# Kernel tuning notes

Hardware: AMD Instinct MI355X
Metric: run time of the kernel (lower is better)

Reference implementation:

```python
import jax, jax.numpy as jnp
import numpy as np

# model dims
V, D, C, H, NL, E, EH = 32000, 256, 2, 8, 2, 8, 1024
B, S = 16, 512
DH = D // H
N = B * S


def _pos_encoding(length, d):
    pos = jnp.arange(length)[:, None].astype(jnp.float32)
    div = jnp.exp(jnp.arange(0, d, 2).astype(jnp.float32) * (-np.log(10000.0) / d))
    pe = jnp.zeros((length, d), dtype=jnp.float32)
    pe = pe.at[:, 0::2].set(jnp.sin(pos * div))
    pe = pe.at[:, 1::2].set(jnp.cos(pos * div))
    return pe


def _ln(x, g, b, eps=1e-5):
    mu = x.mean(-1, keepdims=True)
    var = ((x - mu) ** 2).mean(-1, keepdims=True)
    return (x - mu) / jnp.sqrt(var + eps) * g + b


def setup_inputs():
    key = jax.random.key(0)
    ks = jax.random.split(key, 12)
    n = lambda k, shape, s=0.02: (jax.random.normal(k, shape) * s).astype(jnp.float32)
    return dict(
        x=jax.random.randint(ks[0], (B, S), 0, V),
        emb=n(ks[1], (V, D), 0.1),
        in_proj_w=n(ks[2], (NL, 3 * D, D)),
        in_proj_b=jnp.zeros((NL, 3 * D), jnp.float32),
        out_proj_w=n(ks[3], (NL, D, D)),
        out_proj_b=jnp.zeros((NL, D), jnp.float32),
        ln1_g=jnp.ones((NL, D), jnp.float32), ln1_b=jnp.zeros((NL, D), jnp.float32),
        ln2_g=jnp.ones((NL, D), jnp.float32), ln2_b=jnp.zeros((NL, D), jnp.float32),
        gate_w=n(ks[4], (NL, E, D)), gate_b=jnp.zeros((NL, E), jnp.float32),
        w1=n(ks[5], (NL, E, EH, D)), b1=jnp.zeros((NL, E, EH), jnp.float32),
        w2=n(ks[6], (NL, E, D, EH)), b2=jnp.zeros((NL, E, D), jnp.float32),
        fc1_w=n(ks[7], (128, D), 0.1), fc1_b=jnp.zeros((128,), jnp.float32),
        fc2_w=n(ks[8], (C, 128), 0.1), fc2_b=jnp.zeros((C,), jnp.float32),
    )


def reference(x, emb, in_proj_w, in_proj_b, out_proj_w, out_proj_b,
              ln1_g, ln1_b, ln2_g, ln2_b, gate_w, gate_b,
              w1, b1, w2, b2, fc1_w, fc1_b, fc2_w, fc2_b):
    h = emb[x] * np.sqrt(float(D))                       # [B,S,D]
    h = h + _pos_encoding(S, D)[None]
    pad = h.sum(-1) == 0                                 # key padding mask [B,S]
    for l in range(NL):
        # --- multi-head self-attention ---
        qkv = h @ in_proj_w[l].T + in_proj_b[l]          # [B,S,3D]
        q, k, v = jnp.split(qkv, 3, axis=-1)
        q = q.reshape(B, S, H, DH).transpose(0, 2, 1, 3)
        k = k.reshape(B, S, H, DH).transpose(0, 2, 1, 3)
        v = v.reshape(B, S, H, DH).transpose(0, 2, 1, 3)
        sc = jnp.einsum('bhqd,bhkd->bhqk', q, k) / np.sqrt(float(DH))
        sc = jnp.where(pad[:, None, None, :], -1e9, sc)
        a = jax.nn.softmax(sc, axis=-1)
        ctx = jnp.einsum('bhqk,bhkd->bhqd', a, v).transpose(0, 2, 1, 3).reshape(B, S, D)
        attn_out = ctx @ out_proj_w[l].T + out_proj_b[l]
        h = _ln(h + attn_out, ln1_g[l], ln1_b[l])
        # --- top-1 MoE ---
        xf = h.reshape(N, D)
        gwt = jax.nn.softmax(xf @ gate_w[l].T + gate_b[l], axis=-1)  # [N,E]
        top_idx = jnp.argmax(gwt, axis=-1)                # [N]
        top_w = jnp.max(gwt, axis=-1)                     # [N]
        eh = jax.nn.relu(jnp.einsum('nd,ehd->enh', xf, w1[l]) + b1[l][:, None, :])
        ey = jnp.einsum('enh,edh->end', eh, w2[l]) + b2[l][:, None, :]  # [E,N,D]
        sel = ey[top_idx, jnp.arange(N)]                  # gather routed expert output [N,D]
        moe = (top_w[:, None] * sel).reshape(B, S, D)
        h = _ln(h + moe, ln2_g[l], ln2_b[l])
    m = (~pad)[..., None].astype(h.dtype)                 # [B,S,1]
    pooled = (h * m).sum(1) / jnp.clip(m.sum(1), 1.0)     # masked mean pool [B,D]
    z = jax.nn.relu(pooled @ fc1_w.T + fc1_b)
    return z @ fc2_w.T + fc2_b                            # [B,C]
```

## Files before the change

kernel.cpp:

```cpp
#include <hip/hip_runtime.h>
#include <math.h>

#define D_MODEL 256
#define NTOK    8192
#define SEQ     512
#define NB      16
#define NH      8
#define DHEAD   32
#define NE      8
#define EHID    1024
#define CSTRIDE 32

typedef __attribute__((ext_vector_type(8))) short short8;
typedef __attribute__((ext_vector_type(4))) float floatx4;
typedef unsigned short ushort_t;

__device__ __forceinline__ ushort_t bf16r(float f) {
    unsigned int u = __float_as_uint(f);
    u += 0x7fffu + ((u >> 16) & 1u);
    return (ushort_t)(u >> 16);
}
__device__ __forceinline__ float bf2f(ushort_t b) {
    return __uint_as_float(((unsigned)b) << 16);
}

__global__ __launch_bounds__(256) void wconv(
    const float* __restrict__ src, ushort_t* __restrict__ dst, int n)
{
    const int i = (blockIdx.x * 256 + threadIdx.x) * 4;
    if (i < n) {
        float4 v = *(const float4*)(src + i);
        ushort_t o[4] = { bf16r(v.x), bf16r(v.y), bf16r(v.z), bf16r(v.w) };
        *(uint2*)(dst + i) = *(uint2*)o;
    }
}

__global__ __launch_bounds__(256) void embed_kernel(
    const int* __restrict__ x, const float* __restrict__ emb,
    float* __restrict__ h, ushort_t* __restrict__ hb, int* __restrict__ pad)
{
    __shared__ float wred[4];
    const int n = blockIdx.x;
    const int d = threadIdx.x;
    const int wave = d >> 6;
    const int s = n & (SEQ - 1);
    const int tok = x[n];
    float v = emb[tok * D_MODEL + d] * 16.0f;
    const int j = d >> 1;
    const float c = -9.210340371976184f / 256.0f;
    const float div = expf((float)(2 * j) * c);
    const float ang = (float)s * div;
    v += (d & 1) ? cosf(ang) : sinf(ang);
    h[n * D_MODEL + d] = v;
    hb[n * D_MODEL + d] = bf16r(v);
    float sm = v;
    for (int o = 1; o < 64; o <<= 1) sm += __shfl_xor(sm, o);
    if ((d & 63) == 0) wred[wave] = sm;
    __syncthreads();
    if (d == 0) pad[n] = ((wred[0] + wred[1] + wred[2] + wred[3]) == 0.0f) ? 1 : 0;
}

#define GF_RELU    1
#define GF_OUTBF16 2
#define GF_GATHER  4
#define GF_SCATTER 8

__global__ __launch_bounds__(256) void mfma_gemm(
    const ushort_t* __restrict__ A, const ushort_t* __restrict__ Bw,
    const float* __restrict__ bias, void* __restrict__ Cout,
    int M, int N, int K,
    const int* __restrict__ counts,
    const int* __restrict__ perm, const float* __restrict__ topw,
    int flags)
{
    __shared__ ushort_t As[64][72];
    __shared__ ushort_t Bs[64][72];
    const int e = blockIdx.z;
    int cnt, off = 0;
    if (counts) {
        cnt = counts[e * CSTRIDE];
        if ((int)blockIdx.y * 64 >= cnt) return;
        for (int i = 0; i < e; i++) off += counts[i * CSTRIDE];
    } else { cnt = M; }
    const ushort_t* Bp = Bw + (size_t)e * N * K;
    const float* bp = bias + (size_t)e * N;
    const int m0 = blockIdx.y * 64, n0 = blockIdx.x * 64;
    const int tid = threadIdx.x;
    const int sr0 = tid >> 3;
    const int kc0 = (tid & 7) * 8;
    const int r0 = m0 + sr0, r1 = r0 + 32;
    const bool v0 = r0 < cnt, v1 = r1 < cnt;
    size_t a0, a1;
    if (flags & GF_GATHER) {
        a0 = (size_t)perm[off + (v0 ? r0 : 0)];
        a1 = (size_t)perm[off + (v1 ? r1 : 0)];
    } else {
        a0 = (size_t)(off + (v0 ? r0 : 0));
        a1 = (size_t)(off + (v1 ? r1 : 0));
    }
    const ushort_t* Ap0 = A + a0 * K + kc0;
    const ushort_t* Ap1 = A + a1 * K + kc0;
    const ushort_t* Bp0 = Bp + (size_t)(n0 + sr0) * K + kc0;
    const ushort_t* Bp1 = Bp + (size_t)(n0 + sr0 + 32) * K + kc0;
    const int lane = tid & 63, wave = tid >> 6;
    const int wm = (wave & 1) * 32, wn = (wave >> 1) * 32;
    const int fr = lane & 15, fk = (lane >> 4) * 8;
    floatx4 acc[2][2];
#pragma unroll
    for (int i = 0; i < 2; i++)
#pragma unroll
        for (int jj = 0; jj < 2; jj++) acc[i][jj] = (floatx4){0.f, 0.f, 0.f, 0.f};

    for (int k0 = 0; k0 < K; k0 += 64) {
        uint4 av0 = *(const uint4*)(Ap0 + k0);
        uint4 av1 = *(const uint4*)(Ap1 + k0);
        uint4 bv0 = *(const uint4*)(Bp0 + k0);
        uint4 bv1 = *(const uint4*)(Bp1 + k0);
        __syncthreads();
        *(uint4*)&As[sr0][kc0]      = av0;
        *(uint4*)&As[sr0 + 32][kc0] = av1;
        *(uint4*)&Bs[sr0][kc0]      = bv0;
        *(uint4*)&Bs[sr0 + 32][kc0] = bv1;
        __syncthreads();
#pragma unroll
        for (int ks = 0; ks < 2; ks++) {
            const int ko = ks * 32 + fk;
            short8 fa0 = *(const short8*)&As[wm + fr][ko];
            short8 fa1 = *(const short8*)&As[wm + 16 + fr][ko];
            short8 fb0 = *(const short8*)&Bs[wn + fr][ko];
            short8 fb1 = *(const short8*)&Bs[wn + 16 + fr][ko];
            acc[0][0] = __builtin_amdgcn_mfma_f32_16x16x32_bf16(fa0, fb0, acc[0][0], 0, 0, 0);
            acc[0][1] = __builtin_amdgcn_mfma_f32_16x16x32_bf16(fa0, fb1, acc[0][1], 0, 0, 0);
            acc[1][0] = __builtin_amdgcn_mfma_f32_16x16x32_bf16(fa1, fb0, acc[1][0], 0, 0, 0);
            acc[1][1] = __builtin_amdgcn_mfma_f32_16x16x32_bf16(fa1, fb1, acc[1][1], 0, 0, 0);
        }
    }
    const int crow0 = (lane >> 4) * 4;
    const int ccol = lane & 15;
#pragma unroll
    for (int fm = 0; fm < 2; fm++) {
#pragma unroll
        for (int fn = 0; fn < 2; fn++) {
            const int gcol = n0 + wn + fn * 16 + ccol;
            const float bsv = bp[gcol];
#pragma unroll
            for (int r = 0; r < 4; r++) {
                const int grow = m0 + wm + fm * 16 + crow0 + r;
                if (grow >= cnt) continue;
                float v = acc[fm][fn][r] + bsv;
                if (flags & GF_RELU) v = fmaxf(v, 0.f);
                if (flags & GF_SCATTER) {
                    const int tok = perm[off + grow];
                    ((float*)Cout)[(size_t)tok * N + gcol] = v * topw[tok];
                } else if (flags & GF_OUTBF16) {
                    ((ushort_t*)Cout)[(size_t)(off + grow) * N + gcol] = bf16r(v);
                } else {
                    ((float*)Cout)[(size_t)(off + grow) * N + gcol] = v;
                }
            }
        }
    }
}

__global__ __launch_bounds__(256) void attn_kernel(
    const ushort_t* __restrict__ qkvb, const int* __restrict__ pad,
    ushort_t* __restrict__ ctxb)
{
    __shared__ ushort_t Kt[64 * 40];
    __shared__ ushort_t Vt[32 * 72];
    __shared__ ushort_t Ps[64 * 72];
    __shared__ float padf[512];
    const int tid = threadIdx.x;
    const int lane = tid & 63;
    const int wave = tid >> 6;
    const int quad = lane >> 4;
    const int l16  = lane & 15;
    const int bid = blockIdx.x;
    const int qt = bid & 7;
    const int hh = (bid >> 3) & 7;
    const int b = bid >> 6;
    const int q0 = wave * 16;

    padf[tid]       = (float)pad[b * SEQ + tid];
    padf[tid + 256] = (float)pad[b * SEQ + 256 + tid];

    short8 qfrag = *(const short8*)(qkvb +
        (size_t)(b * SEQ + qt * 64 + q0 + l16) * 768 + hh * 32 + quad * 8);

    const int skey = tid >> 2;
    const int schunk = (tid & 3) * 8;

    floatx4 o0 = {0.f,0.f,0.f,0.f}, o1 = {0.f,0.f,0.f,0.f};
    float lsum[4] = {0.f, 0.f, 0.f, 0.f};
    const float scale = 0.17677669529663687f;

    for (int t = 0; t < 8; t++) {
        const int kbase = b * SEQ + t * 64;
        __syncthreads();
        uint4 kv = *(const uint4*)(qkvb + (size_t)(kbase + skey) * 768 + 256 + hh * 32 + schunk);
        *(uint4*)&Kt[skey * 40 + schunk] = kv;
        uint4 vv = *(const uint4*)(qkvb + (size_t)(kbase + skey) * 768 + 512 + hh * 32 + schunk);
        ushort_t vs[8]; *(uint4*)vs = vv;
#pragma unroll
        for (int j = 0; j < 8; j++) {
            const int d = schunk + j;
            Vt[d * 72 + (skey ^ ((d >> 3) << 3))] = vs[j];
        }
        __syncthreads();
        floatx4 sfr[4];
#pragma unroll
        for (int fn = 0; fn < 4; fn++) {
            short8 kf = *(const short8*)&Kt[(fn * 16 + l16) * 40 + quad * 8];
            sfr[fn] = __builtin_amdgcn_mfma_f32_16x16x32_bf16(
                qfrag, kf, (floatx4){0.f,0.f,0.f,0.f}, 0, 0, 0);
        }
#pragma unroll
        for (int fn = 0; fn < 4; fn++) {
            const int keyl = fn * 16 + l16;
            const float pv = padf[t * 64 + keyl];
#pragma unroll
            for (int r = 0; r < 4; r++) {
                float p = (pv != 0.f) ? 0.f : __expf(sfr[fn][r] * scale);
                ushort_t pb = bf16r(p);
                lsum[r] += bf2f(pb);
                Ps[(q0 + quad * 4 + r) * 72 + keyl] = pb;
            }
        }
#pragma unroll
        for (int kc = 0; kc < 2; kc++) {
            short8 pf = *(const short8*)&Ps[(q0 + l16) * 72 + kc * 32 + quad * 8];
            {
                const int d = l16;
                short8 vf = *(const short8*)&Vt[d * 72 + ((kc * 32 + quad * 8) ^ ((d >> 3) << 3))];
                o0 = __builtin_amdgcn_mfma_f32_16x16x32_bf16(pf, vf, o0, 0, 0, 0);
            }
            {
                const int d = 16 + l16;
                short8 vf = *(const short8*)&Vt[d * 72 + ((kc * 32 + quad * 8) ^ ((d >> 3) << 3))];
                o1 = __builtin_amdgcn_mfma_f32_16x16x32_bf16(pf, vf, o1, 0, 0, 0);
            }
        }
    }
#pragma unroll
    for (int r = 0; r < 4; r++) {
        float v = lsum[r];
        v += __shfl_xor(v, 1); v += __shfl_xor(v, 2);
        v += __shfl_xor(v, 4); v += __shfl_xor(v, 8);
        lsum[r] = 1.f / v;
    }
    const int nq = b * SEQ + qt * 64 + q0 + quad * 4;
#pragma unroll
    for (int r = 0; r < 4; r++) {
        ushort_t* outp = ctxb + (size_t)(nq + r) * 256 + hh * 32;
        outp[l16]      = bf16r(o0[r] * lsum[r]);
        outp[16 + l16] = bf16r(o1[r] * lsum[r]);
    }
}

__global__ __launch_bounds__(256) void add_ln(
    float* __restrict__ h, const float* __restrict__ add,
    const float* __restrict__ g, const float* __restrict__ b,
    ushort_t* __restrict__ hb)
{
    __shared__ float wred[8];
    const int n = blockIdx.x;
    const int d = threadIdx.x;
    const int wave = d >> 6;
    const float v = h[n * D_MODEL + d] + add[n * D_MODEL + d];
    float s = v;
    for (int o = 1; o < 64; o <<= 1) s += __shfl_xor(s, o);
    if ((d & 63) == 0) wred[wave] = s;
    __syncthreads();
    const float mu = (wred[0] + wred[1] + wred[2] + wred[3]) * (1.0f / 256.0f);
    const float c = v - mu;
    float cs = c * c;
    for (int o = 1; o < 64; o <<= 1) cs += __shfl_xor(cs, o);
    if ((d & 63) == 0) wred[4 + wave] = cs;
    __syncthreads();
    const float var = (wred[4] + wred[5] + wred[6] + wred[7]) * (1.0f / 256.0f);
    const float o = c * rsqrtf(var + 1e-5f) * g[d] + b[d];
    h[n * D_MODEL + d] = o;
    hb[n * D_MODEL + d] = bf16r(o);
}

__global__ __launch_bounds__(256) void gate_kernel(
    const float* __restrict__ h, const float* __restrict__ gw,
    const float* __restrict__ gb, int* __restrict__ top_idx,
    float* __restrict__ top_w, int* __restrict__ pos, int* __restrict__ counts)
{
    __shared__ int lidx[128];
    __shared__ int lpos[128];
    __shared__ int hist[NE];
    __shared__ int base[NE];
    const int wave = threadIdx.x >> 6;
    const int lane = threadIdx.x & 63;
    const int t0 = blockIdx.x * 128 + wave * 32;
    float4 gwr[NE];
#pragma unroll
    for (int e = 0; e < NE; e++)
        gwr[e] = *(const float4*)&gw[e * D_MODEL + lane * 4];
    float gbr[NE];
#pragma unroll
    for (int e = 0; e < NE; e++) gbr[e] = gb[e];

    for (int i = 0; i < 32; i++) {
        const int n = t0 + i;
        float4 hv = *(const float4*)&h[(size_t)n * D_MODEL + lane * 4];
        float lg[NE];
#pragma unroll
        for (int e = 0; e < NE; e++)
            lg[e] = hv.x * gwr[e].x + hv.y * gwr[e].y + hv.z * gwr[e].z + hv.w * gwr[e].w;
#pragma unroll
        for (int e = 0; e < NE; e++) {
            float v = lg[e];
            for (int o = 1; o < 64; o <<= 1) v += __shfl_xor(v, o);
            lg[e] = v;
        }
        if (lane == 0) {
            float best = -1e30f; int bi = 0;
#pragma unroll
            for (int e = 0; e < NE; e++) {
                lg[e] += gbr[e];
                if (lg[e] > best) { best = lg[e]; bi = e; }
            }
            float ssum = 0.0f;
#pragma unroll
            for (int e = 0; e < NE; e++) ssum += __expf(lg[e] - best);
            top_idx[n] = bi;
            top_w[n] = 1.0f / ssum;
            lidx[wave * 32 + i] = bi;
        }
    }
    __syncthreads();
    if (threadIdx.x < NE) hist[threadIdx.x] = 0;
    __syncthreads();
    if (threadIdx.x < 128)
        lpos[threadIdx.x] = atomicAdd(&hist[lidx[threadIdx.x]], 1);
    __syncthreads();
    if (threadIdx.x < NE)
        base[threadIdx.x] = atomicAdd(&counts[threadIdx.x * CSTRIDE], hist[threadIdx.x]);
    __syncthreads();
    if (threadIdx.x < 128)
        pos[blockIdx.x * 128 + threadIdx.x] = base[lidx[threadIdx.x]] + lpos[threadIdx.x];
}

__global__ __launch_bounds__(256) void scatter_perm(
    const int* __restrict__ top_idx, const int* __restrict__ pos,
    const int* __restrict__ counts, int* __restrict__ perm)
{
    __shared__ int offs_s[NE];
    if (threadIdx.x < NE) {
        int a = 0;
        for (int i = 0; i < (int)threadIdx.x; i++) a += counts[i * CSTRIDE];
        offs_s[threadIdx.x] = a;
    }
    __syncthreads();
    const int n = blockIdx.x * 256 + threadIdx.x;
    if (n < NTOK) perm[offs_s[top_idx[n]] + pos[n]] = n;
}

__global__ __launch_bounds__(256) void pool1(
    const float* __restrict__ h, const int* __restrict__ pad,
    float* __restrict__ pooled, float* __restrict__ cntb)
{
    const int b = blockIdx.x, c = blockIdx.y, d = threadIdx.x;
    float s = 0.0f; int cnt = 0;
    for (int i = 0; i < 32; i++) {
        const int idx = b * SEQ + c * 32 + i;
        if (!pad[idx]) { s += h[(size_t)idx * D_MODEL + d]; cnt++; }
    }
    atomicAdd(&pooled[b * D_MODEL + d], s);
    if (d == 0) atomicAdd(&cntb[b], (float)cnt);
}

__global__ __launch_bounds__(128) void cls_kernel(
    const float* __restrict__ pooled, const float* __restrict__ cntb,
    const float* __restrict__ fc1w, const float* __restrict__ fc1b,
    const float* __restrict__ fc2w, const float* __restrict__ fc2b,
    float* __restrict__ out)
{
    __shared__ float zs[128];
    const int b = blockIdx.x;
    const int j = threadIdx.x;
    const float invc = 1.0f / fmaxf(cntb[b], 1.0f);
    float s = 0.0f;
    for (int d = 0; d < D_MODEL; d++) s += pooled[b * D_MODEL + d] * fc1w[j * D_MODEL + d];
    zs[j] = fmaxf(s * invc + fc1b[j], 0.0f);
    __syncthreads();
    if (j < 2) {
        float o = fc2b[j];
        for (int i = 0; i < 128; i++) o += zs[i] * fc2w[j * 128 + i];
        out[b * 2 + j] = o;
    }
}

extern "C" void kernel_launch(void* const* d_in, const int* in_sizes, int n_in,
                              void* d_out, int out_size, void* d_ws, size_t ws_size,
                              hipStream_t stream)
{
    const int*   x          = (const int*)d_in[0];
    const float* emb        = (const float*)d_in[1];
    const float* in_proj_w  = (const float*)d_in[2];
    const float* in_proj_b  = (const float*)d_in[3];
    const float* out_proj_w = (const float*)d_in[4];
    const float* out_proj_b = (const float*)d_in[5];
    const float* ln1_g      = (const float*)d_in[6];
    const float* ln1_b      = (const float*)d_in[7];
    const float* ln2_g      = (const float*)d_in[8];
    const float* ln2_b      = (const float*)d_in[9];
    const float* gate_w     = (const float*)d_in[10];
    const float* gate_b     = (const float*)d_in[11];
    const float* w1         = (const float*)d_in[12];
    const float* b1         = (const float*)d_in[13];
    const float* w2         = (const float*)d_in[14];
    const float* b2         = (const float*)d_in[15];
    const float* fc1_w      = (const float*)d_in[16];
    const float* fc1_b      = (const float*)d_in[17];
    const float* fc2_w      = (const float*)d_in[18];
    const float* fc2_b      = (const float*)d_in[19];
    float* out = (float*)d_out;

    float* ws = (float*)d_ws;
    float*    h      = ws;
    float*    tmp    = ws + 2097152;
    ushort_t* qkvb   = (ushort_t*)(ws + 4194304);
    ushort_t* ctxb   = (ushort_t*)(ws + 7340032);
    ushort_t* ehb    = (ushort_t*)(ws + 4194304);
    ushort_t* hb     = (ushort_t*)(ws + 8388608);
    ushort_t* wb     = (ushort_t*)(ws + 9437184);
    float*    top_w  = ws + 10485760;
    float*    pooled = ws + 10493952;
    float*    cntb   = ws + 10498048;
    int* ipart   = (int*)(ws + 10498064);
    int* pad     = ipart;
    int* top_idx = ipart + 8192;
    int* pos     = ipart + 16384;
    int* perm    = ipart + 24576;
    int* counts  = ipart + 32768;

    embed_kernel<<<NTOK, 256, 0, stream>>>(x, emb, h, hb, pad);
    hipMemsetAsync(pooled, 0, (NB * D_MODEL + NB) * sizeof(float), stream);

    for (int l = 0; l < 2; l++) {
        wconv<<<192, 256, 0, stream>>>(in_proj_w + (size_t)l * 196608, wb, 196608);
        mfma_gemm<<<dim3(768 / 64, NTOK / 64, 1), 256, 0, stream>>>(
            hb, wb, in_proj_b + l * 768, qkvb, NTOK, 768, 256,
            nullptr, nullptr, nullptr, GF_OUTBF16);
        attn_kernel<<<NB * NH * (SEQ / 64), 256, 0, stream>>>(qkvb, pad, ctxb);
        wconv<<<64, 256, 0, stream>>>(out_proj_w + (size_t)l * 65536, wb, 65536);
        mfma_gemm<<<dim3(256 / 64, NTOK / 64, 1), 256, 0, stream>>>(
            ctxb, wb, out_proj_b + l * 256, tmp, NTOK, 256, 256,
            nullptr, nullptr, nullptr, 0);
        add_ln<<<NTOK, 256, 0, stream>>>(h, tmp, ln1_g + l * 256, ln1_b + l * 256, hb);
        hipMemsetAsync(counts, 0, NE * CSTRIDE * sizeof(int), stream);
        gate_kernel<<<NTOK / 128, 256, 0, stream>>>(
            h, gate_w + l * NE * 256, gate_b + l * NE, top_idx, top_w, pos, counts);
        scatter_perm<<<NTOK / 256, 256, 0, stream>>>(top_idx, pos, counts, perm);
        wconv<<<2048, 256, 0, stream>>>(w1 + (size_t)l * 2097152, wb, 2097152);
        mfma_gemm<<<dim3(EHID / 64, NTOK / 64, NE), 256, 0, stream>>>(
            hb, wb, b1 + l * NE * EHID, ehb, 0, EHID, 256,
            counts, perm, nullptr, GF_GATHER | GF_RELU | GF_OUTBF16);
        wconv<<<2048, 256, 0, stream>>>(w2 + (size_t)l * 2097152, wb, 2097152);
        mfma_gemm<<<dim3(D_MODEL / 64, NTOK / 64, NE), 256, 0, stream>>>(
            ehb, wb, b2 + l * NE * 256, tmp, 0, D_MODEL, 1024,
            counts, perm, top_w, GF_SCATTER);
        add_ln<<<NTOK, 256, 0, stream>>>(h, tmp, ln2_g + l * 256, ln2_b + l * 256, hb);
    }

    pool1<<<dim3(NB, 16), 256, 0, stream>>>(h, pad, pooled, cntb);
    cls_kernel<<<NB, 128, 0, stream>>>(pooled, cntb, fc1_w, fc1_b, fc2_w, fc2_b, out);
}
```

Baseline: 466.9 us.

## Batch all weight conversions into one launch and enlarge GEMM tiles

All bf16 weight conversions for both layers are merged into one kernel launched at the start, replacing eight small per-GEMM conversion launches that each reused a shared scratch buffer. The MFMA GEMM becomes a template on tile size, and every GEMM now uses 128x128 or 128x64 tiles, so each wave computes more fragments. Larger tiles cut global-load traffic per FLOP and the number of launches, at the cost of more registers and LDS per block, fewer blocks (the QKV GEMM gets 384 blocks), and more wasted rows in sparse expert tiles.

```diff
diff --git a/kernel.cpp b/kernel.cpp
--- a/kernel.cpp
+++ b/kernel.cpp
@@ -24,15 +24,20 @@
     return __uint_as_float(((unsigned)b) << 16);
 }
 
-__global__ __launch_bounds__(256) void wconv(
-    const float* __restrict__ src, ushort_t* __restrict__ dst, int n)
-{
-    const int i = (blockIdx.x * 256 + threadIdx.x) * 4;
-    if (i < n) {
-        float4 v = *(const float4*)(src + i);
-        ushort_t o[4] = { bf16r(v.x), bf16r(v.y), bf16r(v.z), bf16r(v.w) };
-        *(uint2*)(dst + i) = *(uint2*)o;
-    }
+__global__ __launch_bounds__(256) void wconv_all(
+    const float* __restrict__ in_proj_w, const float* __restrict__ out_proj_w,
+    const float* __restrict__ w1, const float* __restrict__ w2,
+    ushort_t* __restrict__ wball)
+{
+    const int g = blockIdx.x * 256 + threadIdx.x;
+    const float* src; ushort_t* dst; int lo;
+    if (g < 98304)        { src = in_proj_w;  dst = wball;           lo = g; }
+    else if (g < 131072)  { src = out_proj_w; dst = wball + 393216;  lo = g - 98304; }
+    else if (g < 1179648) { src = w1;         dst = wball + 524288;  lo = g - 131072; }
+    else                  { src = w2;         dst = wball + 4718592; lo = g - 1179648; }
+    float4 v = *(const float4*)(src + (size_t)lo * 4);
+    ushort_t o[4] = { bf16r(v.x), bf16r(v.y), bf16r(v.z), bf16r(v.w) };
+    *(uint2*)(dst + (size_t)lo * 4) = *(uint2*)o;
 }
 
 __global__ __launch_bounds__(256) void embed_kernel(
@@ -65,7 +70,8 @@
 #define GF_GATHER  4
 #define GF_SCATTER 8
 
-__global__ __launch_bounds__(256) void mfma_gemm(
+template<int BM, int BN>
+__global__ __launch_bounds__(256) void gemm_t(
     const ushort_t* __restrict__ A, const ushort_t* __restrict__ Bw,
     const float* __restrict__ bias, void* __restrict__ Cout,
     int M, int N, int K,
@@ -73,81 +79,84 @@
     const int* __restrict__ perm, const float* __restrict__ topw,
     int flags)
 {
-    __shared__ ushort_t As[64][72];
-    __shared__ ushort_t Bs[64][72];
+    constexpr int MI = BM / 32;
+    constexpr int NI = BN / 32;
+    constexpr int MF = BM / 32;
+    constexpr int NF = BN / 32;
+    __shared__ ushort_t As[BM][72];
+    __shared__ ushort_t Bs[BN][72];
     const int e = blockIdx.z;
     int cnt, off = 0;
     if (counts) {
         cnt = counts[e * CSTRIDE];
-        if ((int)blockIdx.y * 64 >= cnt) return;
+        if ((int)blockIdx.y * BM >= cnt) return;
         for (int i = 0; i < e; i++) off += counts[i * CSTRIDE];
     } else { cnt = M; }
     const ushort_t* Bp = Bw + (size_t)e * N * K;
     const float* bp = bias + (size_t)e * N;
-    const int m0 = blockIdx.y * 64, n0 = blockIdx.x * 64;
+    const int m0 = blockIdx.y * BM, n0 = blockIdx.x * BN;
     const int tid = threadIdx.x;
-    const int sr0 = tid >> 3;
-    const int kc0 = (tid & 7) * 8;
-    const int r0 = m0 + sr0, r1 = r0 + 32;
-    const bool v0 = r0 < cnt, v1 = r1 < cnt;
-    size_t a0, a1;
-    if (flags & GF_GATHER) {
-        a0 = (size_t)perm[off + (v0 ? r0 : 0)];
-        a1 = (size_t)perm[off + (v1 ? r1 : 0)];
-    } else {
-        a0 = (size_t)(off + (v0 ? r0 : 0));
-        a1 = (size_t)(off + (v1 ? r1 : 0));
-    }
-    const ushort_t* Ap0 = A + a0 * K + kc0;
-    const ushort_t* Ap1 = A + a1 * K + kc0;
-    const ushort_t* Bp0 = Bp + (size_t)(n0 + sr0) * K + kc0;
-    const ushort_t* Bp1 = Bp + (size_t)(n0 + sr0 + 32) * K + kc0;
+    const int srow = tid >> 3;
+    const int kc = (tid & 7) * 8;
+    size_t arow[MI];
+#pragma unroll
+    for (int i = 0; i < MI; i++) {
+        const int r = m0 + i * 32 + srow;
+        const bool v = r < cnt;
+        if (flags & GF_GATHER) arow[i] = (size_t)perm[off + (v ? r : 0)];
+        else                   arow[i] = (size_t)(off + (v ? r : 0));
+    }
     const int lane = tid & 63, wave = tid >> 6;
-    const int wm = (wave & 1) * 32, wn = (wave >> 1) * 32;
+    const int wm = (wave & 1) * (BM / 2), wn = (wave >> 1) * (BN / 2);
     const int fr = lane & 15, fk = (lane >> 4) * 8;
-    floatx4 acc[2][2];
-#pragma unroll
-    for (int i = 0; i < 2; i++)
-#pragma unroll
-        for (int jj = 0; jj < 2; jj++) acc[i][jj] = (floatx4){0.f, 0.f, 0.f, 0.f};
+    floatx4 acc[MF][NF];
+#pragma unroll
+    for (int i = 0; i < MF; i++)
+#pragma unroll
+        for (int jj = 0; jj < NF; jj++) acc[i][jj] = (floatx4){0.f, 0.f, 0.f, 0.f};
 
     for (int k0 = 0; k0 < K; k0 += 64) {
-        uint4 av0 = *(const uint4*)(Ap0 + k0);
-        uint4 av1 = *(const uint4*)(Ap1 + k0);
-        uint4 bv0 = *(const uint4*)(Bp0 + k0);
-        uint4 bv1 = *(const uint4*)(Bp1 + k0);
+        uint4 av[MI], bv[NI];
+#pragma unroll
+        for (int i = 0; i < MI; i++)
+            av[i] = *(const uint4*)(A + arow[i] * K + k0 + kc);
+#pragma unroll
+        for (int i = 0; i < NI; i++)
+            bv[i] = *(const uint4*)(Bp + (size_t)(n0 + i * 32 + srow) * K + k0 + kc);
         __syncthreads();
-        *(uint4*)&As[sr0][kc0]      = av0;
-        *(uint4*)&As[sr0 + 32][kc0] = av1;
-        *(uint4*)&Bs[sr0][kc0]      = bv0;
-        *(uint4*)&Bs[sr0 + 32][kc0] = bv1;
+#pragma unroll
+        for (int i = 0; i < MI; i++) *(uint4*)&As[i * 32 + srow][kc] = av[i];
+#pragma unroll
+        for (int i = 0; i < NI; i++) *(uint4*)&Bs[i * 32 + srow][kc] = bv[i];
         __syncthreads();
 #pragma unroll
         for (int ks = 0; ks < 2; ks++) {
             const int ko = ks * 32 + fk;
-            short8 fa0 = *(const short8*)&As[wm + fr][ko];
-            short8 fa1 = *(const short8*)&As[wm + 16 + fr][ko];
-            short8 fb0 = *(const short8*)&Bs[wn + fr][ko];
-            short8 fb1 = *(const short8*)&Bs[wn + 16 + fr][ko];
-            acc[0][0] = __builtin_amdgcn_mfma_f32_16x16x32_bf16(fa0, fb0, acc[0][0], 0, 0, 0);
-            acc[0][1] = __builtin_amdgcn_mfma_f32_16x16x32_bf16(fa0, fb1, acc[0][1], 0, 0, 0);
-            acc[1][0] = __builtin_amdgcn_mfma_f32_16x16x32_bf16(fa1, fb0, acc[1][0], 0, 0, 0);
-            acc[1][1] = __builtin_amdgcn_mfma_f32_16x16x32_bf16(fa1, fb1, acc[1][1], 0, 0, 0);
+            short8 fa[MF], fb[NF];
+#pragma unroll
+            for (int m = 0; m < MF; m++) fa[m] = *(const short8*)&As[wm + m * 16 + fr][ko];
+#pragma unroll
+            for (int n = 0; n < NF; n++) fb[n] = *(const short8*)&Bs[wn + n * 16 + fr][ko];
+#pragma unroll
+            for (int m = 0; m < MF; m++)
+#pragma unroll
+                for (int n = 0; n < NF; n++)
+                    acc[m][n] = __builtin_amdgcn_mfma_f32_16x16x32_bf16(fa[m], fb[n], acc[m][n], 0, 0, 0);
         }
     }
     const int crow0 = (lane >> 4) * 4;
     const int ccol = lane & 15;
 #pragma unroll
-    for (int fm = 0; fm < 2; fm++) {
-#pragma unroll
-        for (int fn = 0; fn < 2; fn++) {
-            const int gcol = n0 + wn + fn * 16 + ccol;
+    for (int m = 0; m < MF; m++) {
+#pragma unroll
+        for (int n = 0; n < NF; n++) {
+            const int gcol = n0 + wn + n * 16 + ccol;
             const float bsv = bp[gcol];
 #pragma unroll
             for (int r = 0; r < 4; r++) {
-                const int grow = m0 + wm + fm * 16 + crow0 + r;
+                const int grow = m0 + wm + m * 16 + crow0 + r;
                 if (grow >= cnt) continue;
-                float v = acc[fm][fn][r] + bsv;
+                float v = acc[m][n][r] + bsv;
                 if (flags & GF_RELU) v = fmaxf(v, 0.f);
                 if (flags & GF_SCATTER) {
                     const int tok = perm[off + grow];
@@ -427,7 +436,6 @@
     ushort_t* ctxb   = (ushort_t*)(ws + 7340032);
     ushort_t* ehb    = (ushort_t*)(ws + 4194304);
     ushort_t* hb     = (ushort_t*)(ws + 8388608);
-    ushort_t* wb     = (ushort_t*)(ws + 9437184);
     float*    top_w  = ws + 10485760;
     float*    pooled = ws + 10493952;
     float*    cntb   = ws + 10498048;
@@ -437,32 +445,35 @@
     int* pos     = ipart + 16384;
     int* perm    = ipart + 24576;
     int* counts  = ipart + 32768;
-
+    ushort_t* wball = (ushort_t*)(ws + 10531088);
+
+    wconv_all<<<8704, 256, 0, stream>>>(in_proj_w, out_proj_w, w1, w2, wball);
     embed_kernel<<<NTOK, 256, 0, stream>>>(x, emb, h, hb, pad);
     hipMemsetAsync(pooled, 0, (NB * D_MODEL + NB) * sizeof(float), stream);
 
     for (int l = 0; l < 2; l++) {
-        wconv<<<192, 256, 0, stream>>>(in_proj_w + (size_t)l * 196608, wb, 196608);
-        mfma_gemm<<<dim3(768 / 64, NTOK / 64, 1), 256, 0, stream>>>(
-            hb, wb, in_proj_b + l * 768, qkvb, NTOK, 768, 256,
+        const ushort_t* inb_l  = wball + (size_t)l * 196608;
+        const ushort_t* outb_l = wball + 393216 + (size_t)l * 65536;
+        const ushort_t* w1b_l  = wball + 524288 + (size_t)l * 2097152;
+        const ushort_t* w2b_l  = wball + 4718592 + (size_t)l * 2097152;
+
+        gemm_t<128, 128><<<dim3(768 / 128, NTOK / 128, 1), 256, 0, stream>>>(
+            hb, inb_l, in_proj_b + l * 768, qkvb, NTOK, 768, 256,
             nullptr, nullptr, nullptr, GF_OUTBF16);
         attn_kernel<<<NB * NH * (SEQ / 64), 256, 0, stream>>>(qkvb, pad, ctxb);
-        wconv<<<64, 256, 0, stream>>>(out_proj_w + (size_t)l * 65536, wb, 65536);
-        mfma_gemm<<<dim3(256 / 64, NTOK / 64, 1), 256, 0, stream>>>(
-            ctxb, wb, out_proj_b + l * 256, tmp, NTOK, 256, 256,
+        gemm_t<128, 64><<<dim3(256 / 64, NTOK / 128, 1), 256, 0, stream>>>(
+            ctxb, outb_l, out_proj_b + l * 256, tmp, NTOK, 256, 256,
             nullptr, nullptr, nullptr, 0);
         add_ln<<<NTOK, 256, 0, stream>>>(h, tmp, ln1_g + l * 256, ln1_b + l * 256, hb);
         hipMemsetAsync(counts, 0, NE * CSTRIDE * sizeof(int), stream);
         gate_kernel<<<NTOK / 128, 256, 0, stream>>>(
             h, gate_w + l * NE * 256, gate_b + l * NE, top_idx, top_w, pos, counts);
         scatter_perm<<<NTOK / 256, 256, 0, stream>>>(top_idx, pos, counts, perm);
-        wconv<<<2048, 256, 0, stream>>>(w1 + (size_t)l * 2097152, wb, 2097152);
-        mfma_gemm<<<dim3(EHID / 64, NTOK / 64, NE), 256, 0, stream>>>(
-            hb, wb, b1 + l * NE * EHID, ehb, 0, EHID, 256,
+        gemm_t<128, 128><<<dim3(EHID / 128, NTOK / 128, NE), 256, 0, stream>>>(
+            hb, w1b_l, b1 + l * NE * EHID, ehb, 0, EHID, 256,
             counts, perm, nullptr, GF_GATHER | GF_RELU | GF_OUTBF16);
-        wconv<<<2048, 256, 0, stream>>>(w2 + (size_t)l * 2097152, wb, 2097152);
-        mfma_gemm<<<dim3(D_MODEL / 64, NTOK / 64, NE), 256, 0, stream>>>(
-            ehb, wb, b2 + l * NE * 256, tmp, 0, D_MODEL, 1024,
+        gemm_t<128, 64><<<dim3(D_MODEL / 64, NTOK / 128, NE), 256, 0, stream>>>(
+            ehb, w2b_l, b2 + l * NE * 256, tmp, 0, D_MODEL, 1024,
             counts, perm, top_w, GF_SCATTER);
         add_ln<<<NTOK, 256, 0, stream>>>(h, tmp, ln2_g + l * 256, ln2_b + l * 256, hb);
     }
```

Result: slower. 827.5 us (+77.2%).
